# Optimization experiments

Hardware: AMD Instinct MI355X
Metric: run time of the kernel (lower is better)

The kernel has to match this reference:

```python
import jax, jax.numpy as jnp
import numpy as np
import math

DIM = 1024
NUM_HEADS = 16


def setup_inputs() -> dict:
    key = jax.random.key(0)
    ks = jax.random.split(key, 6)
    B, S, D = 2, 2048, DIM
    return {
        "q": jax.random.normal(ks[0], (B, S, D), dtype=jnp.float32),
        "k": jax.random.normal(ks[1], (B, S, D), dtype=jnp.float32),
        "v": jax.random.normal(ks[2], (B, S, D), dtype=jnp.float32),
        "wq": jax.random.normal(ks[3], (D, D), dtype=jnp.float32),
        "wk": jax.random.normal(ks[4], (D, D), dtype=jnp.float32),
        "wv": jax.random.normal(ks[5], (D, D), dtype=jnp.float32),
    }


def reference(q, k, v, wq, wk, wv):
    B, S, D = q.shape
    H = NUM_HEADS
    hd = D // H
    # projections: [B,S,D] @ [D,D]
    qp = (q @ wq).reshape(B, H, S, hd)  # NOTE: direct reshape, as in the original
    kp = (k @ wk).reshape(B, H, S, hd)
    vp = (v @ wv).reshape(B, H, S, hd)
    scale = 1.0 / math.sqrt(D)  # original scales by sqrt(dim), not sqrt(head_dim)
    att = jnp.einsum("bhqd,bhkd->bhqk", qp, kp) * scale  # [B,H,S,S]
    att = jax.nn.softmax(att, axis=-1)
    out = jnp.einsum("bhqk,bhkd->bhqd", att, vp)  # [B,H,S,hd]
    out = out.transpose(0, 2, 1, 3).reshape(B, S, D)
    return out
```

## Files before the change

### kernel.cpp

```cpp
#include <hip/hip_runtime.h>
#include <hip/hip_bf16.h>
#include <stdint.h>

#define DIMD 1024
#define SEQ  2048
#define NH   16
#define MROWS 4096
#define NQ   65536

typedef __bf16 bf16_t;
typedef bf16_t bf16x8 __attribute__((ext_vector_type(8)));
typedef float  f32x4  __attribute__((ext_vector_type(4)));
typedef unsigned short u16;
typedef unsigned short u16x4 __attribute__((ext_vector_type(4)));
typedef unsigned short u16x8 __attribute__((ext_vector_type(8)));
typedef unsigned int   u32;
typedef u32 u32x2 __attribute__((ext_vector_type(2)));

static __device__ __forceinline__ f32x4 mfma16(bf16x8 a, bf16x8 b, f32x4 c) {
    return __builtin_amdgcn_mfma_f32_16x16x32_bf16(a, b, c, 0, 0, 0);
}

static __device__ __forceinline__ float fast_exp2(float x) {
#if __has_builtin(__builtin_amdgcn_exp2f)
    return __builtin_amdgcn_exp2f(x);
#else
    return exp2f(x);
#endif
}

#define GLD16(gsrc, ldst) __builtin_amdgcn_global_load_lds(                    \
    (const __attribute__((address_space(1))) unsigned int*)(gsrc),             \
    (__attribute__((address_space(3))) unsigned int*)(ldst), 16, 0, 0)

static __device__ __forceinline__ void split_bf16(float x, u16& h, u16& l) {
    u32 u = __float_as_uint(x);
    u16 hu = (u16)(u >> 16);
    float xh = __uint_as_float((u32)hu << 16);
    float lo = x - xh;
    h = hu;
    l = (u16)(__float_as_uint(lo) >> 16);
}

static __device__ __forceinline__ u32 pack_bf16(float a, float b) {
    return (__float_as_uint(a) >> 16) | (__float_as_uint(b) & 0xffff0000u);
}
static __device__ __forceinline__ u32 pack_bf16_rn(float a, float b) {
    u32 ua = __float_as_uint(a) + 0x8000u;
    u32 ub = __float_as_uint(b) + 0x8000u;
    return (ua >> 16) | (ub & 0xffff0000u);
}
static __device__ __forceinline__ float bf_to_f(u16 v) {
    return __uint_as_float((u32)v << 16);
}

__global__ __launch_bounds__(256) void transWs3(
    const float* __restrict__ w0, const float* __restrict__ w1, const float* __restrict__ w2,
    u16* __restrict__ WTsH, u16* __restrict__ WTsL) {
    const int z = blockIdx.z;
    const float* W = z == 0 ? w0 : z == 1 ? w1 : w2;
    __shared__ u16 Hs[4096], Ls[4096];
    const int tid = threadIdx.x;
    const int kt = blockIdx.x, nt = blockIdx.y;
    const int n0 = nt * 128, k0 = kt * 32;
    #pragma unroll
    for (int i = 0; i < 4; i++) {
        int f = i * 256 + tid;
        int kr = f >> 5, nc4 = (f & 31) * 4;
        f32x4 w = *(const f32x4*)&W[(size_t)(k0 + kr) * DIMD + n0 + nc4];
        int cc = kr >> 3, e = kr & 7;
        #pragma unroll
        for (int j = 0; j < 4; j++) {
            u16 hh, ll; split_bf16(w[j], hh, ll);
            Hs[cc * 1024 + (nc4 + j) * 8 + e] = hh;
            Ls[cc * 1024 + (nc4 + j) * 8 + e] = ll;
        }
    }
    __syncthreads();
    const size_t base = (size_t)z * (DIMD * DIMD) + (size_t)(nt * 32 + kt) * 4096;
    #pragma unroll
    for (int i = 0; i < 2; i++) {
        int idx = (i * 256 + tid) * 8;
        *(u16x8*)(WTsH + base + idx) = *(const u16x8*)&Hs[idx];
        *(u16x8*)(WTsL + base + idx) = *(const u16x8*)&Ls[idx];
    }
}

__global__ __launch_bounds__(256, 3) void proj6(
    const float* __restrict__ xq, const float* __restrict__ xk, const float* __restrict__ xv,
    const u16* __restrict__ WTsH, const u16* __restrict__ WTsL,
    u16* __restrict__ qh, u16* __restrict__ ql,
    u16* __restrict__ kh, u16* __restrict__ kl,
    u16* __restrict__ vh) {

    const int z = blockIdx.z;
    const float* X = z == 0 ? xq : z == 1 ? xk : xv;
    const u16* BH = WTsH + (size_t)z * (DIMD * DIMD);
    const u16* BL = WTsL + (size_t)z * (DIMD * DIMD);
    u16* outH = z == 0 ? qh : z == 1 ? kh : vh;
    u16* outL = z == 0 ? ql : kl;
    const float oscale = z == 0 ? 0.0450842200278f : 1.0f;

    __shared__ u16 lds[16384];
    u16* AsH = lds;
    u16* AsL = lds + 4096;
    u16* BsH = lds + 8192;
    u16* BsL = lds + 12288;

    const int tid  = threadIdx.x;
    const int lane = tid & 63, wave = tid >> 6;
    const int quad = lane >> 4, l16 = lane & 15;
    const int wy = wave >> 1, wx = wave & 1;
    const int m0 = blockIdx.x * 128;
    const int n0 = blockIdx.y * 128;
    const size_t Bregion0 = (size_t)(blockIdx.y * 32) * 4096;

    f32x4 acc[4][4];
    #pragma unroll
    for (int mt = 0; mt < 4; mt++)
        #pragma unroll
        for (int nt = 0; nt < 4; nt++) acc[mt][nt] = (f32x4)0.0f;

    for (int kt = 0; kt < 32; kt++) {
        const int k0 = kt * 32;
        {
            const size_t rb = Bregion0 + (size_t)kt * 4096;
            int c0 = tid, c1 = 256 + tid;
            GLD16(BH + rb + c0 * 8, &BsH[c0 * 8]);
            GLD16(BH + rb + c1 * 8, &BsH[c1 * 8]);
            GLD16(BL + rb + c0 * 8, &BsL[c0 * 8]);
            GLD16(BL + rb + c1 * 8, &BsL[c1 * 8]);
        }
        #pragma unroll
        for (int i = 0; i < 4; i++) {
            int f = i * 256 + tid;
            int r = f >> 3, c4 = (f & 7) * 4;
            f32x4 a = *(const f32x4*)&X[(size_t)(m0 + r) * DIMD + k0 + c4];
            int cc = c4 >> 3, e = c4 & 7;
            u16x4 h4, l4;
            #pragma unroll
            for (int j = 0; j < 4; j++) {
                u16 hh, ll; split_bf16(a[j], hh, ll);
                h4[j] = hh; l4[j] = ll;
            }
            *(u16x4*)&AsH[(cc * 128 + r) * 8 + e] = h4;
            *(u16x4*)&AsL[(cc * 128 + r) * 8 + e] = l4;
        }
        __syncthreads();

        bf16x8 aH[4], aL[4], bH[4], bL[4];
        #pragma unroll
        for (int mt = 0; mt < 4; mt++) {
            int r = wy * 64 + mt * 16 + l16;
            aH[mt] = *(const bf16x8*)&AsH[(quad * 128 + r) * 8];
            aL[mt] = *(const bf16x8*)&AsL[(quad * 128 + r) * 8];
        }
        #pragma unroll
        for (int nt = 0; nt < 4; nt++) {
            int r = wx * 64 + nt * 16 + l16;
            bH[nt] = *(const bf16x8*)&BsH[(quad * 128 + r) * 8];
            bL[nt] = *(const bf16x8*)&BsL[(quad * 128 + r) * 8];
        }
        #pragma unroll
        for (int mt = 0; mt < 4; mt++)
            #pragma unroll
            for (int nt = 0; nt < 4; nt++) {
                acc[mt][nt] = mfma16(aH[mt], bH[nt], acc[mt][nt]);
                acc[mt][nt] = mfma16(aH[mt], bL[nt], acc[mt][nt]);
                acc[mt][nt] = mfma16(aL[mt], bH[nt], acc[mt][nt]);
            }
        __syncthreads();
    }

    #pragma unroll
    for (int mt = 0; mt < 4; mt++)
        #pragma unroll
        for (int nt = 0; nt < 4; nt++)
            #pragma unroll
            for (int r = 0; r < 4; r++) {
                int row = m0 + wy * 64 + mt * 16 + quad * 4 + r;
                int col = n0 + wx * 64 + nt * 16 + l16;
                u16 hh, ll; split_bf16(acc[mt][nt][r] * oscale, hh, ll);
                outH[(size_t)row * DIMD + col] = hh;
                if (z != 2) outL[(size_t)row * DIMD + col] = ll;
            }
}

__global__ __launch_bounds__(256) void transposeV(
    const u16* __restrict__ vh, u16* __restrict__ vt) {
    __shared__ u16 Ls[64][72];
    const int tid = threadIdx.x;
    const int bh = blockIdx.y;
    const int s0 = blockIdx.x * 64;
    const size_t slab = (size_t)bh * (SEQ * 64);
    #pragma unroll
    for (int i = 0; i < 2; i++) {
        int f = i * 256 + tid;
        int r = f >> 3, c = (f & 7) * 8;
        *(u16x8*)&Ls[r][c] = *(const u16x8*)(vh + slab + (size_t)(s0 + r) * 64 + c);
    }
    __syncthreads();
    #pragma unroll
    for (int i = 0; i < 2; i++) {
        int f = i * 256 + tid;
        int d = f >> 3, j = (f & 7) * 8;
        u16x8 o;
        #pragma unroll
        for (int jj = 0; jj < 8; jj++) o[jj] = Ls[j + jj][d];
        *(u16x8*)(vt + slab + (size_t)d * SEQ + s0 + j) = o;
    }
}

__global__ __launch_bounds__(256, 3) void flash6(
    const u16* __restrict__ qh, const u16* __restrict__ ql,
    const u16* __restrict__ kh, const u16* __restrict__ kl,
    const u16* __restrict__ vt,
    u16* __restrict__ Opart, float* __restrict__ Mpart, float* __restrict__ Lpart) {

    __shared__ u16 KH[64][72], KL[64][72], VTs[64][72];
    __shared__ u16 Ps[4][32][72];

    const int tid  = threadIdx.x;
    const int lane = tid & 63, wv = tid >> 6;
    const int quad = lane >> 4, l16 = lane & 15;
    const int bh = blockIdx.x, z = blockIdx.z;
    const size_t slab = (size_t)bh * (SEQ * 64);
    const int q0 = blockIdx.y * 128 + wv * 32;
    const int jbase = z * 1024;

    bf16x8 qfH[2][2], qfL[2][2];
    #pragma unroll
    for (int mq = 0; mq < 2; mq++) {
        const size_t rb = slab + (size_t)(q0 + mq * 16 + l16) * 64;
        #pragma unroll
        for (int kk = 0; kk < 2; kk++) {
            qfH[mq][kk] = *(const bf16x8*)(qh + rb + kk * 32 + quad * 8);
            qfL[mq][kk] = *(const bf16x8*)(ql + rb + kk * 32 + quad * 8);
        }
    }

    f32x4 O[2][4];
    float M[2] = {-3.0e38f, -3.0e38f}, L[2] = {0.0f, 0.0f};
    #pragma unroll
    for (int mq = 0; mq < 2; mq++)
        #pragma unroll
        for (int nv = 0; nv < 4; nv++) O[mq][nv] = (f32x4)0.0f;

    const int f0 = tid, f1 = 256 + tid;
    const int r0 = f0 >> 3, c0 = (f0 & 7) * 8;
    const int r1 = f1 >> 3, c1 = (f1 & 7) * 8;
    u16x8 s0, s1, s2, s3, s4, s5;

    {
        const int j0 = jbase;
        s0 = *(const u16x8*)(kh + slab + (size_t)(j0 + r0) * 64 + c0);
        s1 = *(const u16x8*)(kh + slab + (size_t)(j0 + r1) * 64 + c1);
        s2 = *(const u16x8*)(kl + slab + (size_t)(j0 + r0) * 64 + c0);
        s3 = *(const u16x8*)(kl + slab + (size_t)(j0 + r1) * 64 + c1);
        s4 = *(const u16x8*)(vt + slab + (size_t)r0 * SEQ + j0 + c0);
        s5 = *(const u16x8*)(vt + slab + (size_t)r1 * SEQ + j0 + c1);
    }
    *(u16x8*)&KH[r0][c0] = s0;  *(u16x8*)&KH[r1][c1] = s1;
    *(u16x8*)&KL[r0][c0] = s2;  *(u16x8*)&KL[r1][c1] = s3;
    *(u16x8*)&VTs[r0][c0] = s4; *(u16x8*)&VTs[r1][c1] = s5;
    __syncthreads();

    for (int t = 0; t < 16; t++) {
        if (t < 15) {
            const int j0 = jbase + (t + 1) * 64;
            s0 = *(const u16x8*)(kh + slab + (size_t)(j0 + r0) * 64 + c0);
            s1 = *(const u16x8*)(kh + slab + (size_t)(j0 + r1) * 64 + c1);
            s2 = *(const u16x8*)(kl + slab + (size_t)(j0 + r0) * 64 + c0);
            s3 = *(const u16x8*)(kl + slab + (size_t)(j0 + r1) * 64 + c1);
            s4 = *(const u16x8*)(vt + slab + (size_t)r0 * SEQ + j0 + c0);
            s5 = *(const u16x8*)(vt + slab + (size_t)r1 * SEQ + j0 + c1);
        }

        f32x4 St[2][4];
        #pragma unroll
        for (int mq = 0; mq < 2; mq++)
            #pragma unroll
            for (int nt = 0; nt < 4; nt++) St[mq][nt] = (f32x4)0.0f;
        #pragma unroll
        for (int nt = 0; nt < 4; nt++) {
            const int rB = nt * 16 + l16;
            #pragma unroll
            for (int kk = 0; kk < 2; kk++) {
                bf16x8 kHf = *(const bf16x8*)&KH[rB][kk * 32 + quad * 8];
                bf16x8 kLf = *(const bf16x8*)&KL[rB][kk * 32 + quad * 8];
                #pragma unroll
                for (int mq = 0; mq < 2; mq++) {
                    St[mq][nt] = mfma16(kHf, qfH[mq][kk], St[mq][nt]);
                    St[mq][nt] = mfma16(kLf, qfH[mq][kk], St[mq][nt]);
                    St[mq][nt] = mfma16(kHf, qfL[mq][kk], St[mq][nt]);
                }
            }
        }

        #pragma unroll
        for (int mq = 0; mq < 2; mq++) {
            float mx = St[mq][0][0];
            #pragma unroll
            for (int nt = 0; nt < 4; nt++)
                #pragma unroll
                for (int r = 0; r < 4; r++) mx = fmaxf(mx, St[mq][nt][r]);
            mx = fmaxf(mx, __shfl_xor(mx, 16));
            mx = fmaxf(mx, __shfl_xor(mx, 32));
            float Mn = M[mq];
            if (__any(mx > Mn)) {
                Mn = fmaxf(Mn, mx);
                float al = fast_exp2(M[mq] - Mn);
                M[mq] = Mn;
                L[mq] *= al;
                #pragma unroll
                for (int nv = 0; nv < 4; nv++) O[mq][nv] *= al;
            }
            float rs = 0.0f;
            #pragma unroll
            for (int nt = 0; nt < 4; nt++)
                #pragma unroll
                for (int r = 0; r < 4; r++) {
                    float p = fast_exp2(St[mq][nt][r] - Mn);
                    St[mq][nt][r] = p;
                    rs += p;
                }
            rs += __shfl_xor(rs, 16);
            rs += __shfl_xor(rs, 32);
            L[mq] += rs;
            #pragma unroll
            for (int nt = 0; nt < 4; nt++) {
                u32x2 d;
                d[0] = pack_bf16(St[mq][nt][0], St[mq][nt][1]);
                d[1] = pack_bf16(St[mq][nt][2], St[mq][nt][3]);
                *(u32x2*)&Ps[wv][mq * 16 + l16][nt * 16 + quad * 4] = d;
            }
        }

        #pragma unroll
        for (int kk = 0; kk < 2; kk++) {
            bf16x8 pB[2];
            #pragma unroll
            for (int mq = 0; mq < 2; mq++)
                pB[mq] = *(const bf16x8*)&Ps[wv][mq * 16 + l16][kk * 32 + quad * 8];
            #pragma unroll
            for (int nv = 0; nv < 4; nv++) {
                bf16x8 vF = *(const bf16x8*)&VTs[nv * 16 + l16][kk * 32 + quad * 8];
                #pragma unroll
                for (int mq = 0; mq < 2; mq++)
                    O[mq][nv] = mfma16(vF, pB[mq], O[mq][nv]);
            }
        }

        __syncthreads();
        if (t < 15) {
            *(u16x8*)&KH[r0][c0] = s0;  *(u16x8*)&KH[r1][c1] = s1;
            *(u16x8*)&KL[r0][c0] = s2;  *(u16x8*)&KL[r1][c1] = s3;
            *(u16x8*)&VTs[r0][c0] = s4; *(u16x8*)&VTs[r1][c1] = s5;
        }
        __syncthreads();
    }

    const int qgb = bh * SEQ + q0;
    #pragma unroll
    for (int mq = 0; mq < 2; mq++) {
        const int qg = qgb + mq * 16 + l16;
        #pragma unroll
        for (int nv = 0; nv < 4; nv++) {
            u32x2 d;
            d[0] = pack_bf16_rn(O[mq][nv][0], O[mq][nv][1]);
            d[1] = pack_bf16_rn(O[mq][nv][2], O[mq][nv][3]);
            *(u32x2*)(Opart + ((size_t)(z * NQ + qg)) * 64 + nv * 16 + quad * 4) = d;
        }
        if (quad == 0) {
            Mpart[z * NQ + qg] = M[mq];
            Lpart[z * NQ + qg] = L[mq];
        }
    }
}

__global__ __launch_bounds__(256) void combineK(
    const u16* __restrict__ Opart, const float* __restrict__ Mpart,
    const float* __restrict__ Lpart, float* __restrict__ out) {
    int idx = blockIdx.x * 256 + threadIdx.x;
    int qg = idx >> 4, c4 = (idx & 15) * 4;
    float M0 = Mpart[qg], M1 = Mpart[NQ + qg];
    float L0 = Lpart[qg], L1 = Lpart[NQ + qg];
    float Ms = fmaxf(M0, M1);
    float w0 = fast_exp2(M0 - Ms), w1 = fast_exp2(M1 - Ms);
    float inv = 1.0f / (w0 * L0 + w1 * L1);
    u16x4 a = *(const u16x4*)&Opart[(size_t)qg * 64 + c4];
    u16x4 b = *(const u16x4*)&Opart[((size_t)NQ + qg) * 64 + c4];
    f32x4 o;
    #pragma unroll
    for (int j = 0; j < 4; j++)
        o[j] = (w0 * bf_to_f(a[j]) + w1 * bf_to_f(b[j])) * inv;
    int bh = qg >> 11, s = qg & 2047;
    int bb = bh >> 4, h = bh & 15;
    *(f32x4*)&out[((size_t)(bb * SEQ + s)) * DIMD + h * 64 + c4] = o;
}

extern "C" void kernel_launch(void* const* d_in, const int* in_sizes, int n_in,
                              void* d_out, int out_size, void* d_ws, size_t ws_size,
                              hipStream_t stream) {
    const float* q  = (const float*)d_in[0];
    const float* k  = (const float*)d_in[1];
    const float* v  = (const float*)d_in[2];
    const float* wq = (const float*)d_in[3];
    const float* wk = (const float*)d_in[4];
    const float* wv = (const float*)d_in[5];
    float* out = (float*)d_out;

    char* ws = (char*)d_ws;
    const size_t MB = 1 << 20;
    u16* qh   = (u16*)(ws + 0 * MB);
    u16* ql   = (u16*)(ws + 8 * MB);
    u16* kh   = (u16*)(ws + 16 * MB);
    u16* kl   = (u16*)(ws + 24 * MB);
    u16* vh   = (u16*)(ws + 32 * MB);
    u16* vt   = (u16*)(ws + 40 * MB);
    u16* WTsH = (u16*)(ws + 48 * MB);
    u16* WTsL = (u16*)(ws + 54 * MB);
    u16*   Opart = (u16*)(ws + 48 * MB);
    float* Mpart = (float*)(ws + 64 * MB);
    float* Lpart = (float*)(ws + 64 * MB + 512 * 1024);

    transWs3<<<dim3(32, 8, 3), 256, 0, stream>>>(wq, wk, wv, WTsH, WTsL);

    proj6<<<dim3(32, 8, 3), 256, 0, stream>>>(
        q, k, v, WTsH, WTsL, qh, ql, kh, kl, vh);

    transposeV<<<dim3(SEQ / 64, 2 * NH), 256, 0, stream>>>(vh, vt);

    flash6<<<dim3(2 * NH, SEQ / 128, 2), 256, 0, stream>>>(
        qh, ql, kh, kl, vt, Opart, Mpart, Lpart);

    combineK<<<dim3(NQ * 16 / 256), 256, 0, stream>>>(Opart, Mpart, Lpart, out);
}
```

Measured before the change: 267.3 us.

## Pre-split X into bf16 hi/lo tiles, drop V lo term, enlarge flash query tile

A new splitX kernel converts the fp32 inputs once into hi/lo bf16 tiles laid out for the projection, so proj7 can load A by async global-to-LDS copies instead of converting it per block. For the V projection, proj7 skips the low-part A loads and the aL*bH MFMA term, which removes some precision. The flash kernel now gives each wave 64 query rows and processes each 64-key tile in two 32-key sub-steps, so every K/V tile loaded into LDS is reused across more queries. The trade-offs are an extra kernel with its own round trip through memory, a larger workspace, lower occupancy (launch bounds drop from 3 to 2), and more register pressure.

New measurement: 442.6 us. 65.6% more time.

```diff
diff --git a/kernel.cpp b/kernel.cpp
--- a/kernel.cpp
+++ b/kernel.cpp
@@ -86,15 +86,54 @@
     }
 }
 
-__global__ __launch_bounds__(256, 3) void proj6(
+__global__ __launch_bounds__(256) void splitX(
     const float* __restrict__ xq, const float* __restrict__ xk, const float* __restrict__ xv,
+    u16* __restrict__ XqH, u16* __restrict__ XqL,
+    u16* __restrict__ XkH, u16* __restrict__ XkL,
+    u16* __restrict__ XvH) {
+    const int z = blockIdx.z;
+    const float* X = z == 0 ? xq : z == 1 ? xk : xv;
+    u16* outH = z == 0 ? XqH : z == 1 ? XkH : XvH;
+    u16* outL = z == 0 ? XqL : XkL;
+    __shared__ u16 Hs[4096], Ls[4096];
+    const int tid = threadIdx.x;
+    const int kt = blockIdx.x, mt = blockIdx.y;
+    #pragma unroll
+    for (int i = 0; i < 4; i++) {
+        int f = i * 256 + tid;
+        int r = f >> 3, c4 = (f & 7) * 4;
+        f32x4 a = *(const f32x4*)&X[(size_t)(mt * 128 + r) * DIMD + kt * 32 + c4];
+        int cc = c4 >> 3, e = c4 & 7;
+        #pragma unroll
+        for (int j = 0; j < 4; j++) {
+            u16 hh, ll; split_bf16(a[j], hh, ll);
+            Hs[cc * 1024 + r * 8 + e + j] = hh;
+            Ls[cc * 1024 + r * 8 + e + j] = ll;
+        }
+    }
+    __syncthreads();
+    const size_t base = (size_t)(mt * 32 + kt) * 4096;
+    #pragma unroll
+    for (int i = 0; i < 2; i++) {
+        int idx = (i * 256 + tid) * 8;
+        *(u16x8*)(outH + base + idx) = *(const u16x8*)&Hs[idx];
+        if (z != 2)
+            *(u16x8*)(outL + base + idx) = *(const u16x8*)&Ls[idx];
+    }
+}
+
+__global__ __launch_bounds__(256, 3) void proj7(
+    const u16* __restrict__ XqH, const u16* __restrict__ XqL,
+    const u16* __restrict__ XkH, const u16* __restrict__ XkL,
+    const u16* __restrict__ XvH,
     const u16* __restrict__ WTsH, const u16* __restrict__ WTsL,
     u16* __restrict__ qh, u16* __restrict__ ql,
     u16* __restrict__ kh, u16* __restrict__ kl,
     u16* __restrict__ vh) {
 
     const int z = blockIdx.z;
-    const float* X = z == 0 ? xq : z == 1 ? xk : xv;
+    const u16* AH = z == 0 ? XqH : z == 1 ? XkH : XvH;
+    const u16* AL = z == 0 ? XqL : XkL;
     const u16* BH = WTsH + (size_t)z * (DIMD * DIMD);
     const u16* BL = WTsL + (size_t)z * (DIMD * DIMD);
     u16* outH = z == 0 ? qh : z == 1 ? kh : vh;
@@ -113,6 +152,7 @@
     const int wy = wave >> 1, wx = wave & 1;
     const int m0 = blockIdx.x * 128;
     const int n0 = blockIdx.y * 128;
+    const size_t Aregion0 = (size_t)(blockIdx.x * 32) * 4096;
     const size_t Bregion0 = (size_t)(blockIdx.y * 32) * 4096;
 
     f32x4 acc[4][4];
@@ -121,31 +161,21 @@
         #pragma unroll
         for (int nt = 0; nt < 4; nt++) acc[mt][nt] = (f32x4)0.0f;
 
+    const int c0 = tid * 8, c1 = (256 + tid) * 8;
+
     for (int kt = 0; kt < 32; kt++) {
-        const int k0 = kt * 32;
-        {
-            const size_t rb = Bregion0 + (size_t)kt * 4096;
-            int c0 = tid, c1 = 256 + tid;
-            GLD16(BH + rb + c0 * 8, &BsH[c0 * 8]);
-            GLD16(BH + rb + c1 * 8, &BsH[c1 * 8]);
-            GLD16(BL + rb + c0 * 8, &BsL[c0 * 8]);
-            GLD16(BL + rb + c1 * 8, &BsL[c1 * 8]);
-        }
-        #pragma unroll
-        for (int i = 0; i < 4; i++) {
-            int f = i * 256 + tid;
-            int r = f >> 3, c4 = (f & 7) * 4;
-            f32x4 a = *(const f32x4*)&X[(size_t)(m0 + r) * DIMD + k0 + c4];
-            int cc = c4 >> 3, e = c4 & 7;
-            u16x4 h4, l4;
-            #pragma unroll
-            for (int j = 0; j < 4; j++) {
-                u16 hh, ll; split_bf16(a[j], hh, ll);
-                h4[j] = hh; l4[j] = ll;
-            }
-            *(u16x4*)&AsH[(cc * 128 + r) * 8 + e] = h4;
-            *(u16x4*)&AsL[(cc * 128 + r) * 8 + e] = l4;
-        }
+        const size_t rbA = Aregion0 + (size_t)kt * 4096;
+        const size_t rbB = Bregion0 + (size_t)kt * 4096;
+        GLD16(AH + rbA + c0, &AsH[c0]);
+        GLD16(AH + rbA + c1, &AsH[c1]);
+        if (z != 2) {
+            GLD16(AL + rbA + c0, &AsL[c0]);
+            GLD16(AL + rbA + c1, &AsL[c1]);
+        }
+        GLD16(BH + rbB + c0, &BsH[c0]);
+        GLD16(BH + rbB + c1, &BsH[c1]);
+        GLD16(BL + rbB + c0, &BsL[c0]);
+        GLD16(BL + rbB + c1, &BsL[c1]);
         __syncthreads();
 
         bf16x8 aH[4], aL[4], bH[4], bL[4];
@@ -153,7 +183,7 @@
         for (int mt = 0; mt < 4; mt++) {
             int r = wy * 64 + mt * 16 + l16;
             aH[mt] = *(const bf16x8*)&AsH[(quad * 128 + r) * 8];
-            aL[mt] = *(const bf16x8*)&AsL[(quad * 128 + r) * 8];
+            if (z != 2) aL[mt] = *(const bf16x8*)&AsL[(quad * 128 + r) * 8];
         }
         #pragma unroll
         for (int nt = 0; nt < 4; nt++) {
@@ -161,14 +191,24 @@
             bH[nt] = *(const bf16x8*)&BsH[(quad * 128 + r) * 8];
             bL[nt] = *(const bf16x8*)&BsL[(quad * 128 + r) * 8];
         }
-        #pragma unroll
-        for (int mt = 0; mt < 4; mt++)
-            #pragma unroll
-            for (int nt = 0; nt < 4; nt++) {
-                acc[mt][nt] = mfma16(aH[mt], bH[nt], acc[mt][nt]);
-                acc[mt][nt] = mfma16(aH[mt], bL[nt], acc[mt][nt]);
-                acc[mt][nt] = mfma16(aL[mt], bH[nt], acc[mt][nt]);
-            }
+        if (z != 2) {
+            #pragma unroll
+            for (int mt = 0; mt < 4; mt++)
+                #pragma unroll
+                for (int nt = 0; nt < 4; nt++) {
+                    acc[mt][nt] = mfma16(aH[mt], bH[nt], acc[mt][nt]);
+                    acc[mt][nt] = mfma16(aH[mt], bL[nt], acc[mt][nt]);
+                    acc[mt][nt] = mfma16(aL[mt], bH[nt], acc[mt][nt]);
+                }
+        } else {
+            #pragma unroll
+            for (int mt = 0; mt < 4; mt++)
+                #pragma unroll
+                for (int nt = 0; nt < 4; nt++) {
+                    acc[mt][nt] = mfma16(aH[mt], bH[nt], acc[mt][nt]);
+                    acc[mt][nt] = mfma16(aH[mt], bL[nt], acc[mt][nt]);
+                }
+        }
         __syncthreads();
     }
 
@@ -211,26 +251,26 @@
     }
 }
 
-__global__ __launch_bounds__(256, 3) void flash6(
+__global__ __launch_bounds__(256, 2) void flash7(
     const u16* __restrict__ qh, const u16* __restrict__ ql,
     const u16* __restrict__ kh, const u16* __restrict__ kl,
     const u16* __restrict__ vt,
     u16* __restrict__ Opart, float* __restrict__ Mpart, float* __restrict__ Lpart) {
 
     __shared__ u16 KH[64][72], KL[64][72], VTs[64][72];
-    __shared__ u16 Ps[4][32][72];
+    __shared__ u16 Ps[4][64][40];
 
     const int tid  = threadIdx.x;
     const int lane = tid & 63, wv = tid >> 6;
     const int quad = lane >> 4, l16 = lane & 15;
     const int bh = blockIdx.x, z = blockIdx.z;
     const size_t slab = (size_t)bh * (SEQ * 64);
-    const int q0 = blockIdx.y * 128 + wv * 32;
+    const int q0 = blockIdx.y * 256 + wv * 64;
     const int jbase = z * 1024;
 
-    bf16x8 qfH[2][2], qfL[2][2];
-    #pragma unroll
-    for (int mq = 0; mq < 2; mq++) {
+    bf16x8 qfH[4][2], qfL[4][2];
+    #pragma unroll
+    for (int mq = 0; mq < 4; mq++) {
         const size_t rb = slab + (size_t)(q0 + mq * 16 + l16) * 64;
         #pragma unroll
         for (int kk = 0; kk < 2; kk++) {
@@ -239,16 +279,17 @@
         }
     }
 
-    f32x4 O[2][4];
-    float M[2] = {-3.0e38f, -3.0e38f}, L[2] = {0.0f, 0.0f};
-    #pragma unroll
-    for (int mq = 0; mq < 2; mq++)
+    f32x4 O[4][4];
+    float M[4], L[4];
+    #pragma unroll
+    for (int mq = 0; mq < 4; mq++) { M[mq] = -3.0e38f; L[mq] = 0.0f; }
+    #pragma unroll
+    for (int mq = 0; mq < 4; mq++)
         #pragma unroll
         for (int nv = 0; nv < 4; nv++) O[mq][nv] = (f32x4)0.0f;
 
-    const int f0 = tid, f1 = 256 + tid;
-    const int r0 = f0 >> 3, c0 = (f0 & 7) * 8;
-    const int r1 = f1 >> 3, c1 = (f1 & 7) * 8;
+    const int r0 = tid >> 3, c0 = (tid & 7) * 8;
+    const int r1 = (256 + tid) >> 3, c1 = ((256 + tid) & 7) * 8;
     u16x8 s0, s1, s2, s3, s4, s5;
 
     {
@@ -276,77 +317,77 @@
             s5 = *(const u16x8*)(vt + slab + (size_t)r1 * SEQ + j0 + c1);
         }
 
-        f32x4 St[2][4];
-        #pragma unroll
-        for (int mq = 0; mq < 2; mq++)
-            #pragma unroll
-            for (int nt = 0; nt < 4; nt++) St[mq][nt] = (f32x4)0.0f;
-        #pragma unroll
-        for (int nt = 0; nt < 4; nt++) {
-            const int rB = nt * 16 + l16;
-            #pragma unroll
-            for (int kk = 0; kk < 2; kk++) {
-                bf16x8 kHf = *(const bf16x8*)&KH[rB][kk * 32 + quad * 8];
-                bf16x8 kLf = *(const bf16x8*)&KL[rB][kk * 32 + quad * 8];
-                #pragma unroll
-                for (int mq = 0; mq < 2; mq++) {
-                    St[mq][nt] = mfma16(kHf, qfH[mq][kk], St[mq][nt]);
-                    St[mq][nt] = mfma16(kLf, qfH[mq][kk], St[mq][nt]);
-                    St[mq][nt] = mfma16(kHf, qfL[mq][kk], St[mq][nt]);
+        #pragma unroll
+        for (int sub = 0; sub < 2; sub++) {
+            f32x4 St[4][2];
+            #pragma unroll
+            for (int mq = 0; mq < 4; mq++)
+                #pragma unroll
+                for (int nt = 0; nt < 2; nt++) St[mq][nt] = (f32x4)0.0f;
+            #pragma unroll
+            for (int nt = 0; nt < 2; nt++) {
+                const int rB = sub * 32 + nt * 16 + l16;
+                #pragma unroll
+                for (int kk = 0; kk < 2; kk++) {
+                    bf16x8 kHf = *(const bf16x8*)&KH[rB][kk * 32 + quad * 8];
+                    bf16x8 kLf = *(const bf16x8*)&KL[rB][kk * 32 + quad * 8];
+                    #pragma unroll
+                    for (int mq = 0; mq < 4; mq++) {
+                        St[mq][nt] = mfma16(kHf, qfH[mq][kk], St[mq][nt]);
+                        St[mq][nt] = mfma16(kLf, qfH[mq][kk], St[mq][nt]);
+                        St[mq][nt] = mfma16(kHf, qfL[mq][kk], St[mq][nt]);
+                    }
                 }
             }
-        }
-
-        #pragma unroll
-        for (int mq = 0; mq < 2; mq++) {
-            float mx = St[mq][0][0];
-            #pragma unroll
-            for (int nt = 0; nt < 4; nt++)
-                #pragma unroll
-                for (int r = 0; r < 4; r++) mx = fmaxf(mx, St[mq][nt][r]);
-            mx = fmaxf(mx, __shfl_xor(mx, 16));
-            mx = fmaxf(mx, __shfl_xor(mx, 32));
-            float Mn = M[mq];
-            if (__any(mx > Mn)) {
-                Mn = fmaxf(Mn, mx);
-                float al = fast_exp2(M[mq] - Mn);
-                M[mq] = Mn;
-                L[mq] *= al;
-                #pragma unroll
-                for (int nv = 0; nv < 4; nv++) O[mq][nv] *= al;
+
+            #pragma unroll
+            for (int mq = 0; mq < 4; mq++) {
+                float mx = St[mq][0][0];
+                #pragma unroll
+                for (int nt = 0; nt < 2; nt++)
+                    #pragma unroll
+                    for (int r = 0; r < 4; r++) mx = fmaxf(mx, St[mq][nt][r]);
+                mx = fmaxf(mx, __shfl_xor(mx, 16));
+                mx = fmaxf(mx, __shfl_xor(mx, 32));
+                float Mn = M[mq];
+                if (__any(mx > Mn)) {
+                    Mn = fmaxf(Mn, mx);
+                    float al = fast_exp2(M[mq] - Mn);
+                    M[mq] = Mn;
+                    L[mq] *= al;
+                    #pragma unroll
+                    for (int nv = 0; nv < 4; nv++) O[mq][nv] *= al;
+                }
+                float rs = 0.0f;
+                #pragma unroll
+                for (int nt = 0; nt < 2; nt++)
+                    #pragma unroll
+                    for (int r = 0; r < 4; r++) {
+                        float p = fast_exp2(St[mq][nt][r] - Mn);
+                        St[mq][nt][r] = p;
+                        rs += p;
+                    }
+                rs += __shfl_xor(rs, 16);
+                rs += __shfl_xor(rs, 32);
+                L[mq] += rs;
+                #pragma unroll
+                for (int nt = 0; nt < 2; nt++) {
+                    u32x2 d;
+                    d[0] = pack_bf16(St[mq][nt][0], St[mq][nt][1]);
+                    d[1] = pack_bf16(St[mq][nt][2], St[mq][nt][3]);
+                    *(u32x2*)&Ps[wv][mq * 16 + l16][nt * 16 + quad * 4] = d;
+                }
             }
-            float rs = 0.0f;
-            #pragma unroll
-            for (int nt = 0; nt < 4; nt++)
-                #pragma unroll
-                for (int r = 0; r < 4; r++) {
-                    float p = fast_exp2(St[mq][nt][r] - Mn);
-                    St[mq][nt][r] = p;
-                    rs += p;
-                }
-            rs += __shfl_xor(rs, 16);
-            rs += __shfl_xor(rs, 32);
-            L[mq] += rs;
-            #pragma unroll
-            for (int nt = 0; nt < 4; nt++) {
-                u32x2 d;
-                d[0] = pack_bf16(St[mq][nt][0], St[mq][nt][1]);
-                d[1] = pack_bf16(St[mq][nt][2], St[mq][nt][3]);
-                *(u32x2*)&Ps[wv][mq * 16 + l16][nt * 16 + quad * 4] = d;
-            }
-        }
-
-        #pragma unroll
-        for (int kk = 0; kk < 2; kk++) {
-            bf16x8 pB[2];
-            #pragma unroll
-            for (int mq = 0; mq < 2; mq++)
-                pB[mq] = *(const bf16x8*)&Ps[wv][mq * 16 + l16][kk * 32 + quad * 8];
+
+            bf16x8 pB[4];
+            #pragma unroll
+            for (int mq = 0; mq < 4; mq++)
+                pB[mq] = *(const bf16x8*)&Ps[wv][mq * 16 + l16][quad * 8];
             #pragma unroll
             for (int nv = 0; nv < 4; nv++) {
-                bf16x8 vF = *(const bf16x8*)&VTs[nv * 16 + l16][kk * 32 + quad * 8];
-                #pragma unroll
-                for (int mq = 0; mq < 2; mq++)
+                bf16x8 vF = *(const bf16x8*)&VTs[nv * 16 + l16][sub * 32 + quad * 8];
+                #pragma unroll
+                for (int mq = 0; mq < 4; mq++)
                     O[mq][nv] = mfma16(vF, pB[mq], O[mq][nv]);
             }
         }
@@ -362,7 +403,7 @@
 
     const int qgb = bh * SEQ + q0;
     #pragma unroll
-    for (int mq = 0; mq < 2; mq++) {
+    for (int mq = 0; mq < 4; mq++) {
         const int qg = qgb + mq * 16 + l16;
         #pragma unroll
         for (int nv = 0; nv < 4; nv++) {
@@ -418,20 +459,27 @@
     u16* kl   = (u16*)(ws + 24 * MB);
     u16* vh   = (u16*)(ws + 32 * MB);
     u16* vt   = (u16*)(ws + 40 * MB);
-    u16* WTsH = (u16*)(ws + 48 * MB);
-    u16* WTsL = (u16*)(ws + 54 * MB);
+    u16* XqH  = (u16*)(ws + 48 * MB);
+    u16* XqL  = (u16*)(ws + 56 * MB);
+    u16* XkH  = (u16*)(ws + 64 * MB);
+    u16* XkL  = (u16*)(ws + 72 * MB);
+    u16* XvH  = (u16*)(ws + 80 * MB);
+    u16* WTsH = (u16*)(ws + 88 * MB);
+    u16* WTsL = (u16*)(ws + 94 * MB);
     u16*   Opart = (u16*)(ws + 48 * MB);
-    float* Mpart = (float*)(ws + 64 * MB);
-    float* Lpart = (float*)(ws + 64 * MB + 512 * 1024);
+    float* Mpart = (float*)(ws + 88 * MB);
+    float* Lpart = (float*)(ws + 88 * MB + 512 * 1024);
 
     transWs3<<<dim3(32, 8, 3), 256, 0, stream>>>(wq, wk, wv, WTsH, WTsL);
 
-    proj6<<<dim3(32, 8, 3), 256, 0, stream>>>(
-        q, k, v, WTsH, WTsL, qh, ql, kh, kl, vh);
+    splitX<<<dim3(32, 32, 3), 256, 0, stream>>>(q, k, v, XqH, XqL, XkH, XkL, XvH);
+
+    proj7<<<dim3(32, 8, 3), 256, 0, stream>>>(
+        XqH, XqL, XkH, XkL, XvH, WTsH, WTsL, qh, ql, kh, kl, vh);
 
     transposeV<<<dim3(SEQ / 64, 2 * NH), 256, 0, stream>>>(vh, vt);
 
-    flash6<<<dim3(2 * NH, SEQ / 128, 2), 256, 0, stream>>>(
+    flash7<<<dim3(2 * NH, SEQ / 256, 2), 256, 0, stream>>>(
         qh, ql, kh, kl, vt, Opart, Mpart, Lpart);
 
     combineK<<<dim3(NQ * 16 / 256), 256, 0, stream>>>(Opart, Mpart, Lpart, out);
```
